# Kernel optimization log

Hardware: AMD Instinct MI355X
Metric: run time of the kernel (lower is better)

Reference implementation:

```python
import jax, jax.numpy as jnp
import numpy as np

N = 8_388_608   # signal length (2^23 complex samples)
K = 257         # complex filter taps (Savory CD filter)


def setup_inputs() -> dict:
    key = jax.random.key(0)
    k1, k2, k3, k4 = jax.random.split(key, 4)
    return {
        "x_r": jax.random.normal(k1, (N,), jnp.float32),
        "x_i": jax.random.normal(k2, (N,), jnp.float32),
        "w_r": jax.random.normal(k3, (K,), jnp.float32),
        "w_i": jax.random.normal(k4, (K,), jnp.float32),
    }


def reference(x_r, x_i, w_r, w_i):
    # Complex 1D 'full' cross-correlation (torch conv1d with padding = K-1):
    #   y_real = x_r * w_r - x_i * w_i
    #   y_imag = x_i * w_r + x_r * w_i
    # Expressed as a single fused 2-in/2-out real conv (same math as the
    # original 4 separate conv1d calls + elementwise recombine).
    M = w_r.shape[0] - 1
    x = jnp.stack([x_r, x_i])[None]                # [1, 2, N]
    w = jnp.stack([
        jnp.stack([w_r, -w_i]),                    # real output channel
        jnp.stack([w_i,  w_r]),                    # imag output channel
    ])                                             # [2, 2, K]
    y = jax.lax.conv_general_dilated(
        x, w, window_strides=(1,), padding=[(M, M)],
        dimension_numbers=("NCH", "OIH", "NCH"),
    )                                              # [1, 2, N+K-1]
    return y[0]                                    # [2, N+K-1]: row 0 = real, row 1 = imag
```

## Files before the change

kernel.cpp:

```cpp
#include <hip/hip_runtime.h>

typedef _Float16 half8 __attribute__((ext_vector_type(8)));
typedef float    f32x4 __attribute__((ext_vector_type(4)));

#define NLEN   8388608
#define KTAPS  257
#define MPAD   256
#define OUTLEN (NLEN + MPAD)
#define TPB    256
#define BT     2048
#define NBLK   ((OUTLEN + BT - 1) / BT)
#define NCH    9
#define XELEM  (BT + 288)
#define XSLOT  (XELEM / 8)
#define XPAD   300
#define AFSLOT (2 * NCH * 64)

__device__ __forceinline__ int swz(int t) { return t ^ ((t >> 3) & 7); }

__device__ __forceinline__ void stage_x(const float* __restrict__ xr,
                                        const float* __restrict__ xi,
                                        half8 (*lx)[XPAD], int xbase, int tid)
{
    const bool interior = (xbase >= 0) && (xbase + 8 * XSLOT <= NLEN);
    if (interior) {
        for (int T = tid; T < XSLOT; T += TPB) {
            const int g = xbase + 8 * T;
            const f32x4 a0 = *(const f32x4*)(xr + g);
            const f32x4 a1 = *(const f32x4*)(xr + g + 4);
            const f32x4 b0 = *(const f32x4*)(xi + g);
            const f32x4 b1 = *(const f32x4*)(xi + g + 4);
            half8 vr, vi;
            #pragma unroll
            for (int e = 0; e < 4; ++e) {
                vr[e]     = (_Float16)a0[e];
                vr[e + 4] = (_Float16)a1[e];
                vi[e]     = (_Float16)b0[e];
                vi[e + 4] = (_Float16)b1[e];
            }
            const int Ts = swz(T);
            lx[0][Ts] = vr;
            lx[1][Ts] = vi;
        }
    } else {
        for (int T = tid; T < XSLOT; T += TPB) {
            const int g = xbase + 8 * T;
            half8 vr, vi;
            #pragma unroll
            for (int e = 0; e < 8; ++e) {
                const int ge = g + e;
                const bool ok = (ge >= 0) && (ge < NLEN);
                vr[e] = (_Float16)(ok ? xr[ge] : 0.0f);
                vi[e] = (_Float16)(ok ? xi[ge] : 0.0f);
            }
            const int Ts = swz(T);
            lx[0][Ts] = vr;
            lx[1][Ts] = vi;
        }
    }
}

__global__ __launch_bounds__(TPB) void build_af(
    const float* __restrict__ wr, const float* __restrict__ wi,
    half8* __restrict__ af)
{
    for (int i = threadIdx.x; i < AFSLOT; i += TPB) {
        const int comp = i / (NCH * 64);
        const int rem  = i % (NCH * 64);
        const int c    = rem >> 6;
        const int l    = rem & 63;
        const int row  = l & 15;
        const int jb   = 32 * c + 8 * (l >> 4);
        const float* wp = comp ? wi : wr;
        half8 v;
        #pragma unroll
        for (int e = 0; e < 8; ++e) {
            const int k = jb + e - row;
            const float f = (k >= 0 && k < KTAPS) ? wp[k] : 0.0f;
            v[e] = (_Float16)f;
        }
        af[i] = v;
    }
}

__global__ __launch_bounds__(TPB, 7) void cconv_ws2(
    const float* __restrict__ xr, const float* __restrict__ xi,
    const half8* __restrict__ af, float* __restrict__ out)
{
    __shared__ half8 lx[2][XPAD];

    const int tid   = threadIdx.x;
    const int wv    = tid >> 6;
    const int lane  = tid & 63;
    const int n15   = lane & 15;
    const int lg    = lane >> 4;
    const int t0    = blockIdx.x * BT;
    const int xbase = t0 - MPAD;

    stage_x(xr, xi, lx, xbase, tid);
    __syncthreads();

    f32x4 accr[2], acci[2];
    #pragma unroll
    for (int t = 0; t < 2; ++t) { accr[t] = (f32x4)0.0f; acci[t] = (f32x4)0.0f; }

    const int sT0 = 64 * wv + 2 * n15 + lg;
    const half8* afr = af + lane;
    const half8* afi = af + NCH * 64 + lane;

    half8 awr = afr[0];
    half8 awi = afi[0];
    #pragma unroll
    for (int c = 0; c < NCH; ++c) {
        const int cn = (c + 1 < NCH) ? c + 1 : 0;
        const half8 nwr = afr[cn * 64];
        const half8 nwi = afi[cn * 64];
        const half8 awin = -awi;
        #pragma unroll
        for (int t = 0; t < 2; ++t) {
            const int Ts = swz(sT0 + 32 * t + 4 * c);
            const half8 br = lx[0][Ts];
            const half8 bi = lx[1][Ts];
            accr[t] = __builtin_amdgcn_mfma_f32_16x16x32_f16(awr,  br, accr[t], 0, 0, 0);
            accr[t] = __builtin_amdgcn_mfma_f32_16x16x32_f16(awin, bi, accr[t], 0, 0, 0);
            acci[t] = __builtin_amdgcn_mfma_f32_16x16x32_f16(awr,  bi, acci[t], 0, 0, 0);
            acci[t] = __builtin_amdgcn_mfma_f32_16x16x32_f16(awi,  br, acci[t], 0, 0, 0);
        }
        awr = nwr; awi = nwi;
    }

    const int obase = t0 + 512 * wv + 16 * n15 + 4 * lg;
    #pragma unroll
    for (int t = 0; t < 2; ++t) {
        const int tbase = t0 + 512 * wv + 256 * t;
        if (tbase < OUTLEN) {
            const int pos = obase + 256 * t;
            *(f32x4*)(out + pos)          = accr[t];
            *(f32x4*)(out + OUTLEN + pos) = acci[t];
        }
    }
}

#define FBT    4096
#define FNBLK  ((OUTLEN + FBT - 1) / FBT)
#define FXSLOT ((FBT + 288) / 8)
#define FXPAD  556

__global__ __launch_bounds__(TPB, 4) void cconv_local(
    const float* __restrict__ xr, const float* __restrict__ xi,
    const float* __restrict__ wr, const float* __restrict__ wi,
    float* __restrict__ out)
{
    __shared__ half8 lx[2][FXPAD];
    __shared__ half8 af[2][NCH][64];

    const int tid   = threadIdx.x;
    const int wv    = tid >> 6;
    const int lane  = tid & 63;
    const int n15   = lane & 15;
    const int lg    = lane >> 4;
    const int t0    = blockIdx.x * FBT;
    const int xbase = t0 - MPAD;

    for (int i = tid; i < AFSLOT; i += TPB) {
        const int comp = i / (NCH * 64);
        const int rem  = i % (NCH * 64);
        const int c    = rem >> 6;
        const int l    = rem & 63;
        const int row  = l & 15;
        const int jb   = 32 * c + 8 * (l >> 4);
        const float* wp = comp ? wi : wr;
        half8 v;
        #pragma unroll
        for (int e = 0; e < 8; ++e) {
            const int k = jb + e - row;
            const float f = (k >= 0 && k < KTAPS) ? wp[k] : 0.0f;
            v[e] = (_Float16)f;
        }
        af[comp][c][l] = v;
    }
    {
        const bool interior = (xbase >= 0) && (xbase + 8 * FXSLOT <= NLEN);
        for (int T = tid; T < FXSLOT; T += TPB) {
            const int g = xbase + 8 * T;
            half8 vr, vi;
            if (interior || (g >= 0 && g + 8 <= NLEN)) {
                const f32x4 a0 = *(const f32x4*)(xr + g);
                const f32x4 a1 = *(const f32x4*)(xr + g + 4);
                const f32x4 b0 = *(const f32x4*)(xi + g);
                const f32x4 b1 = *(const f32x4*)(xi + g + 4);
                #pragma unroll
                for (int e = 0; e < 4; ++e) {
                    vr[e]     = (_Float16)a0[e];
                    vr[e + 4] = (_Float16)a1[e];
                    vi[e]     = (_Float16)b0[e];
                    vi[e + 4] = (_Float16)b1[e];
                }
            } else {
                #pragma unroll
                for (int e = 0; e < 8; ++e) {
                    const int ge = g + e;
                    const bool ok = (ge >= 0) && (ge < NLEN);
                    vr[e] = (_Float16)(ok ? xr[ge] : 0.0f);
                    vi[e] = (_Float16)(ok ? xi[ge] : 0.0f);
                }
            }
            const int Ts = swz(T);
            lx[0][Ts] = vr;
            lx[1][Ts] = vi;
        }
    }
    __syncthreads();

    f32x4 accr[4], acci[4];
    #pragma unroll
    for (int t = 0; t < 4; ++t) { accr[t] = (f32x4)0.0f; acci[t] = (f32x4)0.0f; }

    const int sT0 = 128 * wv + 2 * n15 + lg;

    #pragma unroll
    for (int c = 0; c < NCH; ++c) {
        const half8 awr  = af[0][c][lane];
        const half8 awi  = af[1][c][lane];
        const half8 awin = -awi;
        #pragma unroll
        for (int t = 0; t < 4; ++t) {
            const int Ts = swz(sT0 + 32 * t + 4 * c);
            const half8 br = lx[0][Ts];
            const half8 bi = lx[1][Ts];
            accr[t] = __builtin_amdgcn_mfma_f32_16x16x32_f16(awr,  br, accr[t], 0, 0, 0);
            accr[t] = __builtin_amdgcn_mfma_f32_16x16x32_f16(awin, bi, accr[t], 0, 0, 0);
            acci[t] = __builtin_amdgcn_mfma_f32_16x16x32_f16(awr,  bi, acci[t], 0, 0, 0);
            acci[t] = __builtin_amdgcn_mfma_f32_16x16x32_f16(awi,  br, acci[t], 0, 0, 0);
        }
    }

    const int obase = t0 + 1024 * wv + 16 * n15 + 4 * lg;
    #pragma unroll
    for (int t = 0; t < 4; ++t) {
        const int tbase = t0 + 1024 * wv + 256 * t;
        if (tbase < OUTLEN) {
            const int pos = obase + 256 * t;
            *(f32x4*)(out + pos)          = accr[t];
            *(f32x4*)(out + OUTLEN + pos) = acci[t];
        }
    }
}

extern "C" void kernel_launch(void* const* d_in, const int* in_sizes, int n_in,
                              void* d_out, int out_size, void* d_ws, size_t ws_size,
                              hipStream_t stream) {
    const float* xr = (const float*)d_in[0];
    const float* xi = (const float*)d_in[1];
    const float* wr = (const float*)d_in[2];
    const float* wi = (const float*)d_in[3];
    float* o = (float*)d_out;
    if (ws_size >= (size_t)AFSLOT * 16) {
        build_af<<<1, TPB, 0, stream>>>(wr, wi, (half8*)d_ws);
        cconv_ws2<<<NBLK, TPB, 0, stream>>>(xr, xi, (const half8*)d_ws, o);
    } else {
        cconv_local<<<FNBLK, TPB, 0, stream>>>(xr, xi, wr, wi, o);
    }
}
```

Baseline: 41.56 us.

## Double-buffer LDS across multiple tiles per block to overlap loads with MFMA

Replaces the one-tile-per-block convolution kernel with one that processes four consecutive tiles per block using two LDS buffers. Global loads for the next tile are issued into registers before computing the current tile, then converted and stored into the alternate buffer. This aims to hide global load latency behind MFMA work. It doubles LDS use, lowers the occupancy hint from 7 to 4 and cuts the grid to a quarter, which may reduce latency hiding across waves.

```diff
diff --git a/kernel.cpp b/kernel.cpp
--- a/kernel.cpp
+++ b/kernel.cpp
@@ -9,7 +9,9 @@
 #define OUTLEN (NLEN + MPAD)
 #define TPB    256
 #define BT     2048
-#define NBLK   ((OUTLEN + BT - 1) / BT)
+#define NTILES ((OUTLEN + BT - 1) / BT)
+#define TPT    4
+#define NBLKP  ((NTILES + TPT - 1) / TPT)
 #define NCH    9
 #define XELEM  (BT + 288)
 #define XSLOT  (XELEM / 8)
@@ -17,48 +19,6 @@
 #define AFSLOT (2 * NCH * 64)
 
 __device__ __forceinline__ int swz(int t) { return t ^ ((t >> 3) & 7); }
-
-__device__ __forceinline__ void stage_x(const float* __restrict__ xr,
-                                        const float* __restrict__ xi,
-                                        half8 (*lx)[XPAD], int xbase, int tid)
-{
-    const bool interior = (xbase >= 0) && (xbase + 8 * XSLOT <= NLEN);
-    if (interior) {
-        for (int T = tid; T < XSLOT; T += TPB) {
-            const int g = xbase + 8 * T;
-            const f32x4 a0 = *(const f32x4*)(xr + g);
-            const f32x4 a1 = *(const f32x4*)(xr + g + 4);
-            const f32x4 b0 = *(const f32x4*)(xi + g);
-            const f32x4 b1 = *(const f32x4*)(xi + g + 4);
-            half8 vr, vi;
-            #pragma unroll
-            for (int e = 0; e < 4; ++e) {
-                vr[e]     = (_Float16)a0[e];
-                vr[e + 4] = (_Float16)a1[e];
-                vi[e]     = (_Float16)b0[e];
-                vi[e + 4] = (_Float16)b1[e];
-            }
-            const int Ts = swz(T);
-            lx[0][Ts] = vr;
-            lx[1][Ts] = vi;
-        }
-    } else {
-        for (int T = tid; T < XSLOT; T += TPB) {
-            const int g = xbase + 8 * T;
-            half8 vr, vi;
-            #pragma unroll
-            for (int e = 0; e < 8; ++e) {
-                const int ge = g + e;
-                const bool ok = (ge >= 0) && (ge < NLEN);
-                vr[e] = (_Float16)(ok ? xr[ge] : 0.0f);
-                vi[e] = (_Float16)(ok ? xi[ge] : 0.0f);
-            }
-            const int Ts = swz(T);
-            lx[0][Ts] = vr;
-            lx[1][Ts] = vi;
-        }
-    }
-}
 
 __global__ __launch_bounds__(TPB) void build_af(
     const float* __restrict__ wr, const float* __restrict__ wi,
@@ -83,61 +43,144 @@
     }
 }
 
-__global__ __launch_bounds__(TPB, 7) void cconv_ws2(
+__global__ __launch_bounds__(TPB, 4) void cconv_db(
     const float* __restrict__ xr, const float* __restrict__ xi,
     const half8* __restrict__ af, float* __restrict__ out)
 {
-    __shared__ half8 lx[2][XPAD];
+    __shared__ half8 lx[2][2][XPAD];
 
     const int tid   = threadIdx.x;
     const int wv    = tid >> 6;
     const int lane  = tid & 63;
     const int n15   = lane & 15;
     const int lg    = lane >> 4;
-    const int t0    = blockIdx.x * BT;
-    const int xbase = t0 - MPAD;
-
-    stage_x(xr, xi, lx, xbase, tid);
-    __syncthreads();
-
-    f32x4 accr[2], acci[2];
-    #pragma unroll
-    for (int t = 0; t < 2; ++t) { accr[t] = (f32x4)0.0f; acci[t] = (f32x4)0.0f; }
-
-    const int sT0 = 64 * wv + 2 * n15 + lg;
+    const int T0    = tid;
+    const int T1    = tid + TPB;
+    const bool hasT1 = (T1 < XSLOT);
+    const int tile0 = blockIdx.x * TPT;
+    const int ntile = (NTILES - tile0 < TPT) ? (NTILES - tile0) : TPT;
+
+    const int sT0   = 64 * wv + 2 * n15 + lg;
     const half8* afr = af + lane;
     const half8* afi = af + NCH * 64 + lane;
 
-    half8 awr = afr[0];
-    half8 awi = afi[0];
-    #pragma unroll
-    for (int c = 0; c < NCH; ++c) {
-        const int cn = (c + 1 < NCH) ? c + 1 : 0;
-        const half8 nwr = afr[cn * 64];
-        const half8 nwi = afi[cn * 64];
-        const half8 awin = -awi;
+    f32x4 A0a, A0b, B0a, B0b;
+    f32x4 A1a, A1b, B1a, B1b;
+
+    auto issue_loads = [&](int tile, bool& inter) {
+        const int xbase = tile * BT - MPAD;
+        inter = (xbase >= 0) && (xbase + 8 * XSLOT <= NLEN);
+        if (inter) {
+            const int g0 = xbase + 8 * T0;
+            A0a = *(const f32x4*)(xr + g0);
+            A0b = *(const f32x4*)(xr + g0 + 4);
+            B0a = *(const f32x4*)(xi + g0);
+            B0b = *(const f32x4*)(xi + g0 + 4);
+            if (hasT1) {
+                const int g1 = xbase + 8 * T1;
+                A1a = *(const f32x4*)(xr + g1);
+                A1b = *(const f32x4*)(xr + g1 + 4);
+                B1a = *(const f32x4*)(xi + g1);
+                B1b = *(const f32x4*)(xi + g1 + 4);
+            }
+        }
+    };
+
+    auto write_buf = [&](int buf, int tile, bool inter) {
+        if (inter) {
+            half8 vr, vi;
+            #pragma unroll
+            for (int e = 0; e < 4; ++e) {
+                vr[e] = (_Float16)A0a[e]; vr[e + 4] = (_Float16)A0b[e];
+                vi[e] = (_Float16)B0a[e]; vi[e + 4] = (_Float16)B0b[e];
+            }
+            const int Ts0 = swz(T0);
+            lx[buf][0][Ts0] = vr;
+            lx[buf][1][Ts0] = vi;
+            if (hasT1) {
+                half8 wr2, wi2;
+                #pragma unroll
+                for (int e = 0; e < 4; ++e) {
+                    wr2[e] = (_Float16)A1a[e]; wr2[e + 4] = (_Float16)A1b[e];
+                    wi2[e] = (_Float16)B1a[e]; wi2[e + 4] = (_Float16)B1b[e];
+                }
+                const int Ts1 = swz(T1);
+                lx[buf][0][Ts1] = wr2;
+                lx[buf][1][Ts1] = wi2;
+            }
+        } else {
+            const int xbase = tile * BT - MPAD;
+            for (int s = 0; s < 2; ++s) {
+                const int T = s ? T1 : T0;
+                if (s && !hasT1) break;
+                const int g = xbase + 8 * T;
+                half8 vr, vi;
+                #pragma unroll
+                for (int e = 0; e < 8; ++e) {
+                    const int ge = g + e;
+                    const bool ok = (ge >= 0) && (ge < NLEN);
+                    vr[e] = (_Float16)(ok ? xr[ge] : 0.0f);
+                    vi[e] = (_Float16)(ok ? xi[ge] : 0.0f);
+                }
+                const int Ts = swz(T);
+                lx[buf][0][Ts] = vr;
+                lx[buf][1][Ts] = vi;
+            }
+        }
+    };
+
+    auto compute_store = [&](int buf, int tile) {
+        const half8* bre = &lx[buf][0][0];
+        const half8* bim = &lx[buf][1][0];
+        f32x4 accr[2], acci[2];
+        #pragma unroll
+        for (int t = 0; t < 2; ++t) { accr[t] = (f32x4)0.0f; acci[t] = (f32x4)0.0f; }
+
+        half8 awr = afr[0];
+        half8 awi = afi[0];
+        #pragma unroll
+        for (int c = 0; c < NCH; ++c) {
+            const int cn = (c + 1 < NCH) ? c + 1 : 0;
+            const half8 nwr = afr[cn * 64];
+            const half8 nwi = afi[cn * 64];
+            const half8 awin = -awi;
+            #pragma unroll
+            for (int t = 0; t < 2; ++t) {
+                const int Ts = swz(sT0 + 32 * t + 4 * c);
+                const half8 br = bre[Ts];
+                const half8 bi = bim[Ts];
+                accr[t] = __builtin_amdgcn_mfma_f32_16x16x32_f16(awr,  br, accr[t], 0, 0, 0);
+                accr[t] = __builtin_amdgcn_mfma_f32_16x16x32_f16(awin, bi, accr[t], 0, 0, 0);
+                acci[t] = __builtin_amdgcn_mfma_f32_16x16x32_f16(awr,  bi, acci[t], 0, 0, 0);
+                acci[t] = __builtin_amdgcn_mfma_f32_16x16x32_f16(awi,  br, acci[t], 0, 0, 0);
+            }
+            awr = nwr; awi = nwi;
+        }
+
+        const int t0    = tile * BT;
+        const int obase = t0 + 512 * wv + 16 * n15 + 4 * lg;
         #pragma unroll
         for (int t = 0; t < 2; ++t) {
-            const int Ts = swz(sT0 + 32 * t + 4 * c);
-            const half8 br = lx[0][Ts];
-            const half8 bi = lx[1][Ts];
-            accr[t] = __builtin_amdgcn_mfma_f32_16x16x32_f16(awr,  br, accr[t], 0, 0, 0);
-            accr[t] = __builtin_amdgcn_mfma_f32_16x16x32_f16(awin, bi, accr[t], 0, 0, 0);
-            acci[t] = __builtin_amdgcn_mfma_f32_16x16x32_f16(awr,  bi, acci[t], 0, 0, 0);
-            acci[t] = __builtin_amdgcn_mfma_f32_16x16x32_f16(awi,  br, acci[t], 0, 0, 0);
-        }
-        awr = nwr; awi = nwi;
-    }
-
-    const int obase = t0 + 512 * wv + 16 * n15 + 4 * lg;
-    #pragma unroll
-    for (int t = 0; t < 2; ++t) {
-        const int tbase = t0 + 512 * wv + 256 * t;
-        if (tbase < OUTLEN) {
-            const int pos = obase + 256 * t;
-            *(f32x4*)(out + pos)          = accr[t];
-            *(f32x4*)(out + OUTLEN + pos) = acci[t];
-        }
+            const int tbase = t0 + 512 * wv + 256 * t;
+            if (tbase < OUTLEN) {
+                const int pos = obase + 256 * t;
+                *(f32x4*)(out + pos)          = accr[t];
+                *(f32x4*)(out + OUTLEN + pos) = acci[t];
+            }
+        }
+    };
+
+    bool inter0;
+    issue_loads(tile0, inter0);
+    write_buf(0, tile0, inter0);
+
+    for (int j = 0; j < ntile; ++j) {
+        __syncthreads();
+        const int nj = j + 1;
+        bool interN = false;
+        if (nj < ntile) issue_loads(tile0 + nj, interN);
+        compute_store(j & 1, tile0 + j);
+        if (nj < ntile) write_buf(nj & 1, tile0 + nj, interN);
     }
 }
 
@@ -180,11 +223,10 @@
         af[comp][c][l] = v;
     }
     {
-        const bool interior = (xbase >= 0) && (xbase + 8 * FXSLOT <= NLEN);
         for (int T = tid; T < FXSLOT; T += TPB) {
             const int g = xbase + 8 * T;
             half8 vr, vi;
-            if (interior || (g >= 0 && g + 8 <= NLEN)) {
+            if (g >= 0 && g + 8 <= NLEN) {
                 const f32x4 a0 = *(const f32x4*)(xr + g);
                 const f32x4 a1 = *(const f32x4*)(xr + g + 4);
                 const f32x4 b0 = *(const f32x4*)(xi + g);
@@ -257,7 +299,7 @@
     float* o = (float*)d_out;
     if (ws_size >= (size_t)AFSLOT * 16) {
         build_af<<<1, TPB, 0, stream>>>(wr, wi, (half8*)d_ws);
-        cconv_ws2<<<NBLK, TPB, 0, stream>>>(xr, xi, (const half8*)d_ws, o);
+        cconv_db<<<NBLKP, TPB, 0, stream>>>(xr, xi, (const half8*)d_ws, o);
     } else {
         cconv_local<<<FNBLK, TPB, 0, stream>>>(xr, xi, wr, wi, o);
     }
```

Result: slower. 64.32 us (+54.8%).

## Pre-convert input to fp16 planes in workspace and read MFMA operands directly

Applied to the files above, without the earlier changes.

Adds a separate pass that converts the float32 real and imaginary signals into padded fp16 planes in workspace. The convolution kernel then loads its B operands straight from global memory with no LDS staging, keeping only the filter fragments in LDS. It also splits the complex products into four independent accumulators and combines them at the end, which removes the negated-weight MFMA dependency chain. The cost is an extra kernel launch plus a round trip of fp16 data through HBM, and the kernel only takes this path if the workspace is large enough.

```diff
diff --git a/kernel.cpp b/kernel.cpp
--- a/kernel.cpp
+++ b/kernel.cpp
@@ -1,5 +1,6 @@
 #include <hip/hip_runtime.h>
 
+typedef _Float16 half_t;
 typedef _Float16 half8 __attribute__((ext_vector_type(8)));
 typedef float    f32x4 __attribute__((ext_vector_type(4)));
 
@@ -7,64 +8,22 @@
 #define KTAPS  257
 #define MPAD   256
 #define OUTLEN (NLEN + MPAD)
-#define TPB    256
-#define BT     2048
-#define NBLK   ((OUTLEN + BT - 1) / BT)
+#define NT     32769
 #define NCH    9
-#define XELEM  (BT + 288)
-#define XSLOT  (XELEM / 8)
-#define XPAD   300
 #define AFSLOT (2 * NCH * 64)
-
-__device__ __forceinline__ int swz(int t) { return t ^ ((t >> 3) & 7); }
-
-__device__ __forceinline__ void stage_x(const float* __restrict__ xr,
-                                        const float* __restrict__ xi,
-                                        half8 (*lx)[XPAD], int xbase, int tid)
-{
-    const bool interior = (xbase >= 0) && (xbase + 8 * XSLOT <= NLEN);
-    if (interior) {
-        for (int T = tid; T < XSLOT; T += TPB) {
-            const int g = xbase + 8 * T;
-            const f32x4 a0 = *(const f32x4*)(xr + g);
-            const f32x4 a1 = *(const f32x4*)(xr + g + 4);
-            const f32x4 b0 = *(const f32x4*)(xi + g);
-            const f32x4 b1 = *(const f32x4*)(xi + g + 4);
-            half8 vr, vi;
-            #pragma unroll
-            for (int e = 0; e < 4; ++e) {
-                vr[e]     = (_Float16)a0[e];
-                vr[e + 4] = (_Float16)a1[e];
-                vi[e]     = (_Float16)b0[e];
-                vi[e + 4] = (_Float16)b1[e];
-            }
-            const int Ts = swz(T);
-            lx[0][Ts] = vr;
-            lx[1][Ts] = vi;
-        }
-    } else {
-        for (int T = tid; T < XSLOT; T += TPB) {
-            const int g = xbase + 8 * T;
-            half8 vr, vi;
-            #pragma unroll
-            for (int e = 0; e < 8; ++e) {
-                const int ge = g + e;
-                const bool ok = (ge >= 0) && (ge < NLEN);
-                vr[e] = (_Float16)(ok ? xr[ge] : 0.0f);
-                vi[e] = (_Float16)(ok ? xi[ge] : 0.0f);
-            }
-            const int Ts = swz(T);
-            lx[0][Ts] = vr;
-            lx[1][Ts] = vi;
-        }
-    }
-}
-
-__global__ __launch_bounds__(TPB) void build_af(
+#define PLEN   (OUTLEN + 576)
+#define PSLOT  (PLEN / 8)
+#define PLBYTES ((size_t)PLEN * 2)
+#define AFOFF  (2 * PLBYTES)
+#define WSNEED (AFOFF + (size_t)AFSLOT * 16)
+
+#define MFMA __builtin_amdgcn_mfma_f32_16x16x32_f16
+
+__global__ __launch_bounds__(256) void build_af(
     const float* __restrict__ wr, const float* __restrict__ wi,
     half8* __restrict__ af)
 {
-    for (int i = threadIdx.x; i < AFSLOT; i += TPB) {
+    for (int i = threadIdx.x; i < AFSLOT; i += 256) {
         const int comp = i / (NCH * 64);
         const int rem  = i % (NCH * 64);
         const int c    = rem >> 6;
@@ -83,76 +42,106 @@
     }
 }
 
-__global__ __launch_bounds__(TPB, 7) void cconv_ws2(
+__global__ __launch_bounds__(256) void cvt_planes(
     const float* __restrict__ xr, const float* __restrict__ xi,
+    half_t* __restrict__ pr, half_t* __restrict__ pi)
+{
+    const int idx = blockIdx.x * 256 + threadIdx.x;
+    if (idx >= PSLOT) return;
+    const int g = idx * 8 - MPAD;
+    half8 vr, vi;
+    if (g >= 0 && g + 8 <= NLEN) {
+        const f32x4 a0 = *(const f32x4*)(xr + g);
+        const f32x4 a1 = *(const f32x4*)(xr + g + 4);
+        const f32x4 b0 = *(const f32x4*)(xi + g);
+        const f32x4 b1 = *(const f32x4*)(xi + g + 4);
+        #pragma unroll
+        for (int e = 0; e < 4; ++e) {
+            vr[e]     = (_Float16)a0[e];
+            vr[e + 4] = (_Float16)a1[e];
+            vi[e]     = (_Float16)b0[e];
+            vi[e + 4] = (_Float16)b1[e];
+        }
+    } else {
+        #pragma unroll
+        for (int e = 0; e < 8; ++e) {
+            const int ge = g + e;
+            const bool ok = (ge >= 0) && (ge < NLEN);
+            vr[e] = (_Float16)(ok ? xr[ge] : 0.0f);
+            vi[e] = (_Float16)(ok ? xi[ge] : 0.0f);
+        }
+    }
+    *(half8*)(pr + idx * 8) = vr;
+    *(half8*)(pi + idx * 8) = vi;
+}
+
+__global__ __launch_bounds__(256, 4) void cconv_p2(
+    const half_t* __restrict__ pr, const half_t* __restrict__ pi,
     const half8* __restrict__ af, float* __restrict__ out)
 {
-    __shared__ half8 lx[2][XPAD];
-
-    const int tid   = threadIdx.x;
-    const int wv    = tid >> 6;
-    const int lane  = tid & 63;
-    const int n15   = lane & 15;
-    const int lg    = lane >> 4;
-    const int t0    = blockIdx.x * BT;
-    const int xbase = t0 - MPAD;
-
-    stage_x(xr, xi, lx, xbase, tid);
+    __shared__ half8 afl[AFSLOT];
+
+    const int tid  = threadIdx.x;
+    const int wv   = tid >> 6;
+    const int lane = tid & 63;
+    const int n15  = lane & 15;
+    const int lg   = lane >> 4;
+
+    for (int i = tid; i < AFSLOT; i += 256) afl[i] = af[i];
     __syncthreads();
 
-    f32x4 accr[2], acci[2];
-    #pragma unroll
-    for (int t = 0; t < 2; ++t) { accr[t] = (f32x4)0.0f; acci[t] = (f32x4)0.0f; }
-
-    const int sT0 = 64 * wv + 2 * n15 + lg;
-    const half8* afr = af + lane;
-    const half8* afi = af + NCH * 64 + lane;
-
-    half8 awr = afr[0];
-    half8 awi = afi[0];
+    const int tt0 = blockIdx.x * 8 + wv * 2;
+    const int lane_off = 16 * n15 + 8 * lg;
+    const half_t* prA = pr + (size_t)tt0 * 256 + lane_off;
+    const half_t* piA = pi + (size_t)tt0 * 256 + lane_off;
+
+    f32x4 P0 = (f32x4)0.0f, Q0 = (f32x4)0.0f, R0 = (f32x4)0.0f, S0 = (f32x4)0.0f;
+    f32x4 P1 = (f32x4)0.0f, Q1 = (f32x4)0.0f, R1 = (f32x4)0.0f, S1 = (f32x4)0.0f;
+
     #pragma unroll
     for (int c = 0; c < NCH; ++c) {
-        const int cn = (c + 1 < NCH) ? c + 1 : 0;
-        const half8 nwr = afr[cn * 64];
-        const half8 nwi = afi[cn * 64];
-        const half8 awin = -awi;
-        #pragma unroll
-        for (int t = 0; t < 2; ++t) {
-            const int Ts = swz(sT0 + 32 * t + 4 * c);
-            const half8 br = lx[0][Ts];
-            const half8 bi = lx[1][Ts];
-            accr[t] = __builtin_amdgcn_mfma_f32_16x16x32_f16(awr,  br, accr[t], 0, 0, 0);
-            accr[t] = __builtin_amdgcn_mfma_f32_16x16x32_f16(awin, bi, accr[t], 0, 0, 0);
-            acci[t] = __builtin_amdgcn_mfma_f32_16x16x32_f16(awr,  bi, acci[t], 0, 0, 0);
-            acci[t] = __builtin_amdgcn_mfma_f32_16x16x32_f16(awi,  br, acci[t], 0, 0, 0);
-        }
-        awr = nwr; awi = nwi;
-    }
-
-    const int obase = t0 + 512 * wv + 16 * n15 + 4 * lg;
-    #pragma unroll
-    for (int t = 0; t < 2; ++t) {
-        const int tbase = t0 + 512 * wv + 256 * t;
-        if (tbase < OUTLEN) {
-            const int pos = obase + 256 * t;
-            *(f32x4*)(out + pos)          = accr[t];
-            *(f32x4*)(out + OUTLEN + pos) = acci[t];
-        }
-    }
-}
-
+        const half8 awr = afl[c * 64 + lane];
+        const half8 awi = afl[NCH * 64 + c * 64 + lane];
+        const half8 br0 = *(const half8*)(prA + 32 * c);
+        const half8 bi0 = *(const half8*)(piA + 32 * c);
+        const half8 br1 = *(const half8*)(prA + 32 * c + 256);
+        const half8 bi1 = *(const half8*)(piA + 32 * c + 256);
+        P0 = MFMA(awr, br0, P0, 0, 0, 0);
+        S0 = MFMA(awi, br0, S0, 0, 0, 0);
+        R0 = MFMA(awr, bi0, R0, 0, 0, 0);
+        Q0 = MFMA(awi, bi0, Q0, 0, 0, 0);
+        P1 = MFMA(awr, br1, P1, 0, 0, 0);
+        S1 = MFMA(awi, br1, S1, 0, 0, 0);
+        R1 = MFMA(awr, bi1, R1, 0, 0, 0);
+        Q1 = MFMA(awi, bi1, Q1, 0, 0, 0);
+    }
+
+    const int pos0 = tt0 * 256 + 16 * n15 + 4 * lg;
+    if (tt0 < NT) {
+        *(f32x4*)(out + pos0)          = P0 - Q0;
+        *(f32x4*)(out + OUTLEN + pos0) = R0 + S0;
+    }
+    if (tt0 + 1 < NT) {
+        *(f32x4*)(out + pos0 + 256)          = P1 - Q1;
+        *(f32x4*)(out + OUTLEN + pos0 + 256) = R1 + S1;
+    }
+}
+
+#define FTPB   256
 #define FBT    4096
 #define FNBLK  ((OUTLEN + FBT - 1) / FBT)
 #define FXSLOT ((FBT + 288) / 8)
 #define FXPAD  556
 
-__global__ __launch_bounds__(TPB, 4) void cconv_local(
+__device__ __forceinline__ int fswz(int t) { return t ^ ((t >> 3) & 7); }
+
+__global__ __launch_bounds__(FTPB, 4) void cconv_local(
     const float* __restrict__ xr, const float* __restrict__ xi,
     const float* __restrict__ wr, const float* __restrict__ wi,
     float* __restrict__ out)
 {
     __shared__ half8 lx[2][FXPAD];
-    __shared__ half8 af[2][NCH][64];
+    __shared__ half8 afl[2][NCH][64];
 
     const int tid   = threadIdx.x;
     const int wv    = tid >> 6;
@@ -162,7 +151,7 @@
     const int t0    = blockIdx.x * FBT;
     const int xbase = t0 - MPAD;
 
-    for (int i = tid; i < AFSLOT; i += TPB) {
+    for (int i = tid; i < AFSLOT; i += FTPB) {
         const int comp = i / (NCH * 64);
         const int rem  = i % (NCH * 64);
         const int c    = rem >> 6;
@@ -177,38 +166,35 @@
             const float f = (k >= 0 && k < KTAPS) ? wp[k] : 0.0f;
             v[e] = (_Float16)f;
         }
-        af[comp][c][l] = v;
-    }
-    {
-        const bool interior = (xbase >= 0) && (xbase + 8 * FXSLOT <= NLEN);
-        for (int T = tid; T < FXSLOT; T += TPB) {
-            const int g = xbase + 8 * T;
-            half8 vr, vi;
-            if (interior || (g >= 0 && g + 8 <= NLEN)) {
-                const f32x4 a0 = *(const f32x4*)(xr + g);
-                const f32x4 a1 = *(const f32x4*)(xr + g + 4);
-                const f32x4 b0 = *(const f32x4*)(xi + g);
-                const f32x4 b1 = *(const f32x4*)(xi + g + 4);
-                #pragma unroll
-                for (int e = 0; e < 4; ++e) {
-                    vr[e]     = (_Float16)a0[e];
-                    vr[e + 4] = (_Float16)a1[e];
-                    vi[e]     = (_Float16)b0[e];
-                    vi[e + 4] = (_Float16)b1[e];
-                }
-            } else {
-                #pragma unroll
-                for (int e = 0; e < 8; ++e) {
-                    const int ge = g + e;
-                    const bool ok = (ge >= 0) && (ge < NLEN);
-                    vr[e] = (_Float16)(ok ? xr[ge] : 0.0f);
-                    vi[e] = (_Float16)(ok ? xi[ge] : 0.0f);
-                }
+        afl[comp][c][l] = v;
+    }
+    for (int T = tid; T < FXSLOT; T += FTPB) {
+        const int g = xbase + 8 * T;
+        half8 vr, vi;
+        if (g >= 0 && g + 8 <= NLEN) {
+            const f32x4 a0 = *(const f32x4*)(xr + g);
+            const f32x4 a1 = *(const f32x4*)(xr + g + 4);
+            const f32x4 b0 = *(const f32x4*)(xi + g);
+            const f32x4 b1 = *(const f32x4*)(xi + g + 4);
+            #pragma unroll
+            for (int e = 0; e < 4; ++e) {
+                vr[e]     = (_Float16)a0[e];
+                vr[e + 4] = (_Float16)a1[e];
+                vi[e]     = (_Float16)b0[e];
+                vi[e + 4] = (_Float16)b1[e];
             }
-            const int Ts = swz(T);
-            lx[0][Ts] = vr;
-            lx[1][Ts] = vi;
-        }
+        } else {
+            #pragma unroll
+            for (int e = 0; e < 8; ++e) {
+                const int ge = g + e;
+                const bool ok = (ge >= 0) && (ge < NLEN);
+                vr[e] = (_Float16)(ok ? xr[ge] : 0.0f);
+                vi[e] = (_Float16)(ok ? xi[ge] : 0.0f);
+            }
+        }
+        const int Ts = fswz(T);
+        lx[0][Ts] = vr;
+        lx[1][Ts] = vi;
     }
     __syncthreads();
 
@@ -220,18 +206,18 @@
 
     #pragma unroll
     for (int c = 0; c < NCH; ++c) {
-        const half8 awr  = af[0][c][lane];
-        const half8 awi  = af[1][c][lane];
+        const half8 awr  = afl[0][c][lane];
+        const half8 awi  = afl[1][c][lane];
         const half8 awin = -awi;
         #pragma unroll
         for (int t = 0; t < 4; ++t) {
-            const int Ts = swz(sT0 + 32 * t + 4 * c);
+            const int Ts = fswz(sT0 + 32 * t + 4 * c);
             const half8 br = lx[0][Ts];
             const half8 bi = lx[1][Ts];
-            accr[t] = __builtin_amdgcn_mfma_f32_16x16x32_f16(awr,  br, accr[t], 0, 0, 0);
-            accr[t] = __builtin_amdgcn_mfma_f32_16x16x32_f16(awin, bi, accr[t], 0, 0, 0);
-            acci[t] = __builtin_amdgcn_mfma_f32_16x16x32_f16(awr,  bi, acci[t], 0, 0, 0);
-            acci[t] = __builtin_amdgcn_mfma_f32_16x16x32_f16(awi,  br, acci[t], 0, 0, 0);
+            accr[t] = MFMA(awr,  br, accr[t], 0, 0, 0);
+            accr[t] = MFMA(awin, bi, accr[t], 0, 0, 0);
+            acci[t] = MFMA(awr,  bi, acci[t], 0, 0, 0);
+            acci[t] = MFMA(awi,  br, acci[t], 0, 0, 0);
         }
     }
 
@@ -255,10 +241,14 @@
     const float* wr = (const float*)d_in[2];
     const float* wi = (const float*)d_in[3];
     float* o = (float*)d_out;
-    if (ws_size >= (size_t)AFSLOT * 16) {
-        build_af<<<1, TPB, 0, stream>>>(wr, wi, (half8*)d_ws);
-        cconv_ws2<<<NBLK, TPB, 0, stream>>>(xr, xi, (const half8*)d_ws, o);
+    if (ws_size >= WSNEED) {
+        half_t* pr = (half_t*)d_ws;
+        half_t* pi = (half_t*)((char*)d_ws + PLBYTES);
+        half8*  af = (half8*)((char*)d_ws + AFOFF);
+        build_af<<<1, 256, 0, stream>>>(wr, wi, af);
+        cvt_planes<<<(PSLOT + 255) / 256, 256, 0, stream>>>(xr, xi, pr, pi);
+        cconv_p2<<<(NT + 7) / 8, 256, 0, stream>>>(pr, pi, af, o);
     } else {
-        cconv_local<<<FNBLK, TPB, 0, stream>>>(xr, xi, wr, wi, o);
-    }
-}
+        cconv_local<<<FNBLK, FTPB, 0, stream>>>(xr, xi, wr, wi, o);
+    }
+}
```

Result: slower. 58.27 us (+40.2%).
